# Kernel optimization log

Hardware: AMD Instinct MI355X
Metric: run time of the kernel (lower is better)

Reference implementation:

```python
import jax, jax.numpy as jnp
import numpy as np

EMBED_DIM = 2048
NUM_HEADS = 16
HEAD_DIM = EMBED_DIM // NUM_HEADS
BASE = 10000.0


def rotate_half(x):
    half = x.shape[-1] // 2
    x1, x2 = x[..., :half], x[..., half:]
    return jnp.concatenate([-x2, x1], axis=-1)


def apply_rope(x, base=BASE):
    # x: [B, H, S, Dh]
    S, Dh = x.shape[-2], x.shape[-1]
    inv_freq = 1.0 / (base ** (jnp.arange(0, Dh, 2, dtype=jnp.float32) / Dh))
    t = jnp.arange(S, dtype=jnp.float32)
    freqs = jnp.einsum('i,j->ij', t, inv_freq)          # [S, Dh/2]
    emb = jnp.concatenate([freqs, freqs], axis=-1)      # [S, Dh]
    return x * jnp.cos(emb) + rotate_half(x) * jnp.sin(emb)


def setup_inputs() -> dict:
    key = jax.random.key(0)
    ks = jax.random.split(key, 9)
    B, S, D = 2, 2048, EMBED_DIM
    xavier = lambda k, shape: jax.random.uniform(
        k, shape, jnp.float32, -1.0, 1.0) * float(np.sqrt(6.0 / (shape[0] + shape[1])))
    return {
        'x': jax.random.normal(ks[0], (B, S, D), jnp.float32),
        'q_w': xavier(ks[1], (D, D)),
        'k_w': xavier(ks[2], (D, D)),
        'v_w': xavier(ks[3], (D, D)),
        'q_b': jnp.zeros((D,), jnp.float32),
        'k_b': jnp.zeros((D,), jnp.float32),
        'v_b': jnp.zeros((D,), jnp.float32),
        'out_w': xavier(ks[4], (D, D)),
        'out_b': jnp.zeros((D,), jnp.float32),
    }


def reference(x, q_w, k_w, v_w, q_b, k_b, v_b, out_w, out_b):
    B, S, D = x.shape
    H, Dh = NUM_HEADS, HEAD_DIM
    scaling = Dh ** -0.5
    # F.linear(x, W, b) = x @ W.T + b
    q = (x @ q_w.T + q_b).reshape(B, S, H, Dh).transpose(0, 2, 1, 3)
    k = (x @ k_w.T + k_b).reshape(B, S, H, Dh).transpose(0, 2, 1, 3)
    v = (x @ v_w.T + v_b).reshape(B, S, H, Dh).transpose(0, 2, 1, 3)
    q = apply_rope(q)
    k = apply_rope(k)
    attn = jnp.einsum('bhqd,bhkd->bhqk', q, k) * scaling
    probs = jax.nn.softmax(attn, axis=-1)
    out = jnp.einsum('bhqk,bhkd->bhqd', probs, v)
    out = out.transpose(0, 2, 1, 3).reshape(B, S, D)
    return out @ out_w.T + out_b
```

## Files before the change

### kernel.cpp

```cpp
#include <hip/hip_runtime.h>
#include <stdint.h>

typedef __bf16 bf16;
typedef __bf16 bf16x4 __attribute__((ext_vector_type(4)));
typedef __bf16 bf16x8 __attribute__((ext_vector_type(8)));
typedef float f32x4 __attribute__((ext_vector_type(4)));

#define DM 2048
#define MM 4096
#define MFMA16(a, b, c) __builtin_amdgcn_mfma_f32_16x16x32_bf16(a, b, c, 0, 0, 0)

__device__ __forceinline__ void gload_lds16(const void* g, void* l) {
  __builtin_amdgcn_global_load_lds((const __attribute__((address_space(1))) uint32_t*)g,
                                   (__attribute__((address_space(3))) uint32_t*)l, 16, 0, 0);
}

__global__ __launch_bounds__(256) void cvt_f32_bf16(
    const float* __restrict__ s0, const float* __restrict__ s1,
    const float* __restrict__ s2, const float* __restrict__ s3,
    const float* __restrict__ s4,
    bf16* __restrict__ d0, bf16* __restrict__ d1, bf16* __restrict__ d2,
    bf16* __restrict__ d3, bf16* __restrict__ d4)
{
  const size_t i4 = (size_t)(blockIdx.x * 256 + threadIdx.x) * 4;
  const float* s; bf16* d; size_t off;
  if      (i4 <  8388608u) { s = s0; d = d0; off = i4;             }
  else if (i4 < 12582912u) { s = s1; d = d1; off = i4 -  8388608u; }
  else if (i4 < 16777216u) { s = s2; d = d2; off = i4 - 12582912u; }
  else if (i4 < 20971520u) { s = s3; d = d3; off = i4 - 16777216u; }
  else                     { s = s4; d = d4; off = i4 - 20971520u; }
  const float4 v = *(const float4*)(s + off);
  bf16x4 o = { (bf16)v.x, (bf16)v.y, (bf16)v.z, (bf16)v.w };
  *(bf16x4*)(d + off) = o;
}

__global__ __launch_bounds__(256, 2) void gemm_qkv_fused(
    const bf16* __restrict__ A,
    const bf16* __restrict__ Wq, const bf16* __restrict__ Wk, const bf16* __restrict__ Wv,
    const float* __restrict__ qb, const float* __restrict__ kb, const float* __restrict__ vb,
    bf16* __restrict__ Cq, bf16* __restrict__ Ck, bf16* __restrict__ Cv)
{
  __shared__ __align__(16) bf16 smem[32768];
  bf16* As = smem;
  bf16* Ws = smem + 8192;

  const int id = blockIdx.x;
  const int xcd = id & 7, jj = id >> 3;
  const int n0 = (xcd * 2 + (jj >> 5)) * 128;
  const int m0 = (jj & 31) * 128;

  const int t = threadIdx.x;
  const int wave = t >> 6, lane = t & 63;
  const int quad = lane >> 4, c16 = lane & 15;
  const int wr = wave >> 1, wc = wave & 1;

  f32x4 acc[3][4][4] = {};

  const int srow = t >> 3;
  const int scol = ((t & 7) ^ (srow & 7)) * 8;
  const bf16* gA  = A  + (size_t)(m0 + srow) * DM + scol;
  const bf16* gW0 = Wq + (size_t)(n0 + srow) * DM + scol;
  const bf16* gW1 = Wk + (size_t)(n0 + srow) * DM + scol;
  const bf16* gW2 = Wv + (size_t)(n0 + srow) * DM + scol;

  for (int k0 = 0; k0 < DM; k0 += 64) {
#pragma unroll
    for (int rr = 0; rr < 4; ++rr) {
      const size_t go = (size_t)(rr * 32) * DM;
      const int lo = (rr * 256 + wave * 64) * 8;
      gload_lds16(gA  + go, As + lo);
      gload_lds16(gW0 + go, Ws + lo);
      gload_lds16(gW1 + go, Ws + 8192 + lo);
      gload_lds16(gW2 + go, Ws + 16384 + lo);
    }
    gA += 64; gW0 += 64; gW1 += 64; gW2 += 64;
    __syncthreads();

#pragma unroll
    for (int ks = 0; ks < 2; ++ks) {
      bf16x8 af[4];
#pragma unroll
      for (int i = 0; i < 4; ++i) {
        const int row = wr * 64 + i * 16 + c16;
        const int gi = (ks * 4 + quad) ^ (row & 7);
        af[i] = *(const bf16x8*)&As[row * 64 + gi * 8];
      }
#pragma unroll
      for (int z = 0; z < 3; ++z) {
        bf16x8 bfr[4];
#pragma unroll
        for (int jx = 0; jx < 4; ++jx) {
          const int row = wc * 64 + jx * 16 + c16;
          const int gi = (ks * 4 + quad) ^ (row & 7);
          bfr[jx] = *(const bf16x8*)&Ws[z * 8192 + row * 64 + gi * 8];
        }
#pragma unroll
        for (int i = 0; i < 4; ++i)
#pragma unroll
          for (int jx = 0; jx < 4; ++jx)
            acc[z][i][jx] = MFMA16(af[i], bfr[jx], acc[z][i][jx]);
      }
    }
    __syncthreads();
  }

  const int h = n0 >> 7;
#pragma unroll
  for (int jx = 0; jx < 4; ++jx) {
    const int d = wc * 64 + jx * 16 + c16;
    const float bv = vb[n0 + d];
#pragma unroll
    for (int i = 0; i < 4; ++i) {
      const int row = m0 + wr * 64 + i * 16 + quad * 4;
      const int b = row >> 11, s = row & 2047;
      bf16x4 o;
#pragma unroll
      for (int r = 0; r < 4; ++r) o[r] = (bf16)(acc[2][i][jx][r] + bv);
      *(bf16x4*)&Cv[((size_t)((b * 16 + h) * 128 + d)) * 2048 + s] = o;
    }
  }

  bf16* Tl = smem;
#pragma unroll
  for (int z = 0; z < 2; ++z) {
    __syncthreads();
#pragma unroll
    for (int jx = 0; jx < 4; ++jx) {
      const int col = wc * 64 + jx * 16 + c16;
      const float bv = (z == 0 ? qb : kb)[n0 + col];
#pragma unroll
      for (int i = 0; i < 4; ++i) {
        const int row = wr * 64 + i * 16 + quad * 4;
#pragma unroll
        for (int r = 0; r < 4; ++r)
          Tl[(row + r) * 136 + col] = (bf16)(acc[z][i][jx][r] + bv);
      }
    }
    __syncthreads();
    bf16* C = (z == 0) ? Cq : Ck;
    const float scale = (z == 0) ? 0.08838834764831845f * 1.4426950408889634f : 1.0f;
#pragma unroll
    for (int rr = 0; rr < 4; ++rr) {
      const int row = rr * 32 + (t >> 3);
      const int d0 = (t & 7) * 8;
      const int s = (m0 + row) & 2047;
      bf16x8 xa = *(const bf16x8*)&Tl[row * 136 + d0];
      bf16x8 xb = *(const bf16x8*)&Tl[row * 136 + d0 + 64];
      bf16x8 o1, o2;
#pragma unroll
      for (int j = 0; j < 8; ++j) {
        const float inv_freq = __expf((float)(d0 + j) * -0.14391156514261228f);
        float sn, cs;
        __sincosf((float)s * inv_freq, &sn, &cs);
        const float a = (float)xa[j], bb = (float)xb[j];
        o1[j] = (bf16)((a * cs - bb * sn) * scale);
        o2[j] = (bf16)((bb * cs + a * sn) * scale);
      }
      *(bf16x8*)&C[(size_t)(m0 + row) * DM + n0 + d0]      = o1;
      *(bf16x8*)&C[(size_t)(m0 + row) * DM + n0 + d0 + 64] = o2;
    }
  }
}

__global__ __launch_bounds__(256, 2) void gemm_bias_f32(
    const bf16* __restrict__ A, const bf16* __restrict__ W,
    const float* __restrict__ bias, float* __restrict__ C)
{
  __shared__ __align__(16) bf16 As[8192];
  __shared__ __align__(16) bf16 Bs[8192];
  const int id = blockIdx.x;
  const int xcd = id & 7, jj = id >> 3;
  const int n0 = (xcd * 2 + (jj >> 5)) * 128;
  const int m0 = (jj & 31) * 128;

  const int t = threadIdx.x;
  const int wave = t >> 6, lane = t & 63;
  const int quad = lane >> 4, c16 = lane & 15;
  const int wr = wave >> 1, wc = wave & 1;

  f32x4 acc[4][4] = {};
  const int srow = t >> 3;
  const int scol = ((t & 7) ^ (srow & 7)) * 8;
  const bf16* gA = A + (size_t)(m0 + srow) * DM + scol;
  const bf16* gB = W + (size_t)(n0 + srow) * DM + scol;

  for (int k0 = 0; k0 < DM; k0 += 64) {
#pragma unroll
    for (int rr = 0; rr < 4; ++rr) {
      const size_t go = (size_t)(rr * 32) * DM;
      const int lo = (rr * 256 + wave * 64) * 8;
      gload_lds16(gA + go, As + lo);
      gload_lds16(gB + go, Bs + lo);
    }
    gA += 64; gB += 64;
    __syncthreads();

#pragma unroll
    for (int ks = 0; ks < 2; ++ks) {
      bf16x8 af[4], bfr[4];
#pragma unroll
      for (int i = 0; i < 4; ++i) {
        const int row = wr * 64 + i * 16 + c16;
        const int gi = (ks * 4 + quad) ^ (row & 7);
        af[i] = *(const bf16x8*)&As[row * 64 + gi * 8];
      }
#pragma unroll
      for (int jx = 0; jx < 4; ++jx) {
        const int row = wc * 64 + jx * 16 + c16;
        const int gi = (ks * 4 + quad) ^ (row & 7);
        bfr[jx] = *(const bf16x8*)&Bs[row * 64 + gi * 8];
      }
#pragma unroll
      for (int i = 0; i < 4; ++i)
#pragma unroll
        for (int jx = 0; jx < 4; ++jx)
          acc[i][jx] = MFMA16(af[i], bfr[jx], acc[i][jx]);
    }
    __syncthreads();
  }

#pragma unroll
  for (int jx = 0; jx < 4; ++jx) {
    const int col = n0 + wc * 64 + jx * 16 + c16;
    const float bv = bias[col];
#pragma unroll
    for (int i = 0; i < 4; ++i) {
      const int row = m0 + wr * 64 + i * 16 + quad * 4;
#pragma unroll
      for (int r = 0; r < 4; ++r)
        C[(size_t)(row + r) * DM + col] = acc[i][jx][r] + bv;
    }
  }
}

__global__ __launch_bounds__(256, 2) void attn(
    const bf16* __restrict__ Q, const bf16* __restrict__ K,
    const bf16* __restrict__ Vt, bf16* __restrict__ O)
{
  __shared__ __align__(16) bf16 Ks[2][4][32][32];
  __shared__ __align__(16) bf16 Vs[2][128][32];
  __shared__ __align__(16) bf16 Ps[4][2][16][40];
  const int t = threadIdx.x;
  const int wave = t >> 6, lane = t & 63;
  const int quad = lane >> 4, c16 = lane & 15;
  const int id = blockIdx.x;
  const int xcd = id & 7, jj = id >> 3;
  const int bh = xcd * 4 + (jj >> 4);
  const int q0 = (jj & 15) * 128;
  const int b = bh >> 4, h = bh & 15;

  bf16x8 qf[2][4];
#pragma unroll
  for (int g = 0; g < 2; ++g) {
    const bf16* qrow = Q + (size_t)(b * 2048 + q0 + wave * 32 + g * 16 + c16) * 2048
                         + (size_t)h * 128 + quad * 8;
#pragma unroll
    for (int ks = 0; ks < 4; ++ks) qf[g][ks] = *(const bf16x8*)(qrow + ks * 32);
  }

  float l_i[2] = {0.f, 0.f};
  f32x4 o_acc[2][8] = {};

  const bf16* Kg = K + (size_t)(b * 2048) * 2048 + (size_t)h * 128;
  const bf16* Vg = Vt + (size_t)bh * 128 * 2048;

  auto stage = [&](int kt0, int nb) {
#pragma unroll
    for (int rr = 0; rr < 2; ++rr) {
      const int g = rr * 256 + t;
      const int ks = g >> 7, krow = (g >> 2) & 31, c8 = g & 3;
      gload_lds16(Kg + (size_t)(kt0 + krow) * 2048 + ks * 32 + ((c8 ^ ((krow >> 1) & 3)) * 8),
                  (bf16*)Ks[nb] + (rr * 256 + wave * 64) * 8);
    }
#pragma unroll
    for (int rr = 0; rr < 2; ++rr) {
      const int g = rr * 256 + t;
      const int d = g >> 2, c8 = g & 3;
      gload_lds16(Vg + (size_t)d * 2048 + kt0 + ((c8 ^ ((d >> 1) & 3)) * 8),
                  (bf16*)Vs[nb] + (rr * 256 + wave * 64) * 8);
    }
  };

  stage(0, 0);
  __syncthreads();

#pragma unroll 2
  for (int kt = 0; kt < 64; ++kt) {
    const int cb = kt & 1;
    if (kt < 63) stage((kt + 1) * 32, cb ^ 1);

    f32x4 st[2][2] = {};
#pragma unroll
    for (int ks = 0; ks < 4; ++ks)
#pragma unroll
      for (int nt = 0; nt < 2; ++nt) {
        const int row = nt * 16 + c16;
        bf16x8 kf = *(const bf16x8*)&Ks[cb][ks][row][(quad ^ ((row >> 1) & 3)) * 8];
        st[0][nt] = MFMA16(kf, qf[0][ks], st[0][nt]);
        st[1][nt] = MFMA16(kf, qf[1][ks], st[1][nt]);
      }

#pragma unroll
    for (int g = 0; g < 2; ++g) {
      float ps = 0.f;
#pragma unroll
      for (int nt = 0; nt < 2; ++nt) {
        bf16x4 pk;
#pragma unroll
        for (int r = 0; r < 4; ++r) {
          const float p = exp2f(st[g][nt][r]);
          ps += p;
          pk[r] = (bf16)p;
        }
        *(bf16x4*)&Ps[wave][g][c16][nt * 16 + quad * 4] = pk;
      }
      l_i[g] += ps;
    }

    bf16x8 pf0 = *(const bf16x8*)&Ps[wave][0][c16][quad * 8];
    bf16x8 pf1 = *(const bf16x8*)&Ps[wave][1][c16][quad * 8];
#pragma unroll
    for (int dt = 0; dt < 8; ++dt) {
      const int row = dt * 16 + c16;
      bf16x8 vf = *(const bf16x8*)&Vs[cb][row][(quad ^ ((row >> 1) & 3)) * 8];
      o_acc[0][dt] = MFMA16(vf, pf0, o_acc[0][dt]);
      o_acc[1][dt] = MFMA16(vf, pf1, o_acc[1][dt]);
    }

    __syncthreads();
  }

#pragma unroll
  for (int g = 0; g < 2; ++g) {
    float l = l_i[g];
    l += __shfl_xor(l, 16, 64);
    l += __shfl_xor(l, 32, 64);
    const float invl = 1.0f / l;
    const int qrow = q0 + wave * 32 + g * 16 + c16;
    bf16* orow = O + (size_t)(b * 2048 + qrow) * 2048 + (size_t)h * 128 + quad * 4;
#pragma unroll
    for (int dt = 0; dt < 8; ++dt) {
      bf16x4 o;
#pragma unroll
      for (int r = 0; r < 4; ++r) o[r] = (bf16)(o_acc[g][dt][r] * invl);
      *(bf16x4*)(orow + dt * 16) = o;
    }
  }
}

extern "C" void kernel_launch(void* const* d_in, const int* in_sizes, int n_in,
                              void* d_out, int out_size, void* d_ws, size_t ws_size,
                              hipStream_t stream)
{
  (void)in_sizes; (void)n_in; (void)out_size; (void)ws_size;
  const float* x   = (const float*)d_in[0];
  const float* q_w = (const float*)d_in[1];
  const float* k_w = (const float*)d_in[2];
  const float* v_w = (const float*)d_in[3];
  const float* q_b = (const float*)d_in[4];
  const float* k_b = (const float*)d_in[5];
  const float* v_b = (const float*)d_in[6];
  const float* o_w = (const float*)d_in[7];
  const float* o_b = (const float*)d_in[8];

  const size_t NELEM = (size_t)MM * DM;
  const size_t WELEM = (size_t)DM * DM;
  bf16* Xb  = (bf16*)d_ws;
  bf16* Wq  = Xb + NELEM;
  bf16* Wk  = Wq + WELEM;
  bf16* Wv  = Wk + WELEM;
  bf16* Wo  = Wv + WELEM;
  bf16* Q   = Wo + WELEM;
  bf16* Kb  = Q  + NELEM;
  bf16* Vt  = Kb + NELEM;
  bf16* attnO = Xb;

  cvt_f32_bf16<<<24576, 256, 0, stream>>>(x, q_w, k_w, v_w, o_w, Xb, Wq, Wk, Wv, Wo);

  gemm_qkv_fused<<<512, 256, 0, stream>>>(Xb, Wq, Wk, Wv, q_b, k_b, v_b, Q, Kb, Vt);
  attn<<<512, 256, 0, stream>>>(Q, Kb, Vt, attnO);
  gemm_bias_f32<<<512, 256, 0, stream>>>(attnO, Wo, o_b, (float*)d_out);
}
```

Measured before the change: 369.6 us.

## Switch attention to 32x32 MFMA with register-resident P and 64-key tiles

The attention kernel now uses 32x32x16 bf16 MFMAs instead of 16x16x32, and each wave handles 32 query rows with a single f32x16 accumulator set. The probability tile is packed with v_cvt_pk_bf16_f32 and rearranged across lanes with v_permlane32_swap, which removes the LDS round-trip for P. The key tile grows from 32 to 64 per iteration, halving the number of barriers, and the LDS swizzle changes to match. The larger K/V buffers raise LDS use, and the hand-written lane permutation is a correctness risk.

```diff
diff --git a/kernel.cpp b/kernel.cpp
--- a/kernel.cpp
+++ b/kernel.cpp
@@ -5,10 +5,12 @@
 typedef __bf16 bf16x4 __attribute__((ext_vector_type(4)));
 typedef __bf16 bf16x8 __attribute__((ext_vector_type(8)));
 typedef float f32x4 __attribute__((ext_vector_type(4)));
+typedef float f32x16 __attribute__((ext_vector_type(16)));
 
 #define DM 2048
 #define MM 4096
 #define MFMA16(a, b, c) __builtin_amdgcn_mfma_f32_16x16x32_bf16(a, b, c, 0, 0, 0)
+#define MFMA32(a, b, c) __builtin_amdgcn_mfma_f32_32x32x16_bf16(a, b, c, 0, 0, 0)
 
 __device__ __forceinline__ void gload_lds16(const void* g, void* l) {
   __builtin_amdgcn_global_load_lds((const __attribute__((address_space(1))) uint32_t*)g,
@@ -237,46 +239,44 @@
     const bf16* __restrict__ Q, const bf16* __restrict__ K,
     const bf16* __restrict__ Vt, bf16* __restrict__ O)
 {
-  __shared__ __align__(16) bf16 Ks[2][4][32][32];
-  __shared__ __align__(16) bf16 Vs[2][128][32];
-  __shared__ __align__(16) bf16 Ps[4][2][16][40];
+  __shared__ __align__(16) bf16 Ks[2][64][128];
+  __shared__ __align__(16) bf16 Vs[2][128][64];
   const int t = threadIdx.x;
   const int wave = t >> 6, lane = t & 63;
-  const int quad = lane >> 4, c16 = lane & 15;
+  const int r31 = lane & 31, h = lane >> 5;
   const int id = blockIdx.x;
   const int xcd = id & 7, jj = id >> 3;
   const int bh = xcd * 4 + (jj >> 4);
   const int q0 = (jj & 15) * 128;
-  const int b = bh >> 4, h = bh & 15;
-
-  bf16x8 qf[2][4];
-#pragma unroll
-  for (int g = 0; g < 2; ++g) {
-    const bf16* qrow = Q + (size_t)(b * 2048 + q0 + wave * 32 + g * 16 + c16) * 2048
-                         + (size_t)h * 128 + quad * 8;
-#pragma unroll
-    for (int ks = 0; ks < 4; ++ks) qf[g][ks] = *(const bf16x8*)(qrow + ks * 32);
-  }
-
-  float l_i[2] = {0.f, 0.f};
-  f32x4 o_acc[2][8] = {};
-
-  const bf16* Kg = K + (size_t)(b * 2048) * 2048 + (size_t)h * 128;
+  const int b = bh >> 4, hd = bh & 15;
+
+  bf16x8 qf[8];
+  {
+    const bf16* qrow = Q + (size_t)(b * 2048 + q0 + wave * 32 + r31) * 2048
+                         + (size_t)hd * 128 + h * 8;
+#pragma unroll
+    for (int ks = 0; ks < 8; ++ks) qf[ks] = *(const bf16x8*)(qrow + ks * 16);
+  }
+
+  float l_i = 0.f;
+  f32x16 o_acc[4] = {};
+
+  const bf16* Kg = K + (size_t)(b * 2048) * 2048 + (size_t)hd * 128;
   const bf16* Vg = Vt + (size_t)bh * 128 * 2048;
 
   auto stage = [&](int kt0, int nb) {
 #pragma unroll
-    for (int rr = 0; rr < 2; ++rr) {
-      const int g = rr * 256 + t;
-      const int ks = g >> 7, krow = (g >> 2) & 31, c8 = g & 3;
-      gload_lds16(Kg + (size_t)(kt0 + krow) * 2048 + ks * 32 + ((c8 ^ ((krow >> 1) & 3)) * 8),
+    for (int rr = 0; rr < 4; ++rr) {
+      const int G = rr * 256 + t;
+      const int key = G >> 4, gl = G & 15;
+      gload_lds16(Kg + (size_t)(kt0 + key) * 2048 + ((gl ^ (key & 7)) * 8),
                   (bf16*)Ks[nb] + (rr * 256 + wave * 64) * 8);
     }
 #pragma unroll
-    for (int rr = 0; rr < 2; ++rr) {
-      const int g = rr * 256 + t;
-      const int d = g >> 2, c8 = g & 3;
-      gload_lds16(Vg + (size_t)d * 2048 + kt0 + ((c8 ^ ((d >> 1) & 3)) * 8),
+    for (int rr = 0; rr < 4; ++rr) {
+      const int G = rr * 256 + t;
+      const int d = G >> 3, gl = G & 7;
+      gload_lds16(Vg + (size_t)d * 2048 + kt0 + ((gl ^ (d & 7)) * 8),
                   (bf16*)Vs[nb] + (rr * 256 + wave * 64) * 8);
     }
   };
@@ -285,67 +285,69 @@
   __syncthreads();
 
 #pragma unroll 2
-  for (int kt = 0; kt < 64; ++kt) {
+  for (int kt = 0; kt < 32; ++kt) {
     const int cb = kt & 1;
-    if (kt < 63) stage((kt + 1) * 32, cb ^ 1);
-
-    f32x4 st[2][2] = {};
-#pragma unroll
-    for (int ks = 0; ks < 4; ++ks)
-#pragma unroll
-      for (int nt = 0; nt < 2; ++nt) {
-        const int row = nt * 16 + c16;
-        bf16x8 kf = *(const bf16x8*)&Ks[cb][ks][row][(quad ^ ((row >> 1) & 3)) * 8];
-        st[0][nt] = MFMA16(kf, qf[0][ks], st[0][nt]);
-        st[1][nt] = MFMA16(kf, qf[1][ks], st[1][nt]);
-      }
-
-#pragma unroll
-    for (int g = 0; g < 2; ++g) {
-      float ps = 0.f;
-#pragma unroll
-      for (int nt = 0; nt < 2; ++nt) {
-        bf16x4 pk;
-#pragma unroll
-        for (int r = 0; r < 4; ++r) {
-          const float p = exp2f(st[g][nt][r]);
-          ps += p;
-          pk[r] = (bf16)p;
+    if (kt < 31) stage((kt + 1) * 64, cb ^ 1);
+
+#pragma unroll
+    for (int rb = 0; rb < 2; ++rb) {
+      f32x16 st = {};
+#pragma unroll
+      for (int ks = 0; ks < 8; ++ks) {
+        const int key = rb * 32 + r31;
+        const int g = (2 * ks + h) ^ (key & 7);
+        bf16x8 kf = *(const bf16x8*)&Ks[cb][key][g * 8];
+        st = MFMA32(kf, qf[ks], st);
+      }
+
+      float p[16];
+#pragma unroll
+      for (int r = 0; r < 16; ++r) { p[r] = exp2f(st[r]); l_i += p[r]; }
+
+      uint32_t pka[4], pkb[4];
+#pragma unroll
+      for (int pp = 0; pp < 4; ++pp) {
+        asm("v_cvt_pk_bf16_f32 %0, %1, %2"
+            : "=v"(pka[pp]) : "v"(p[4 * pp + 0]), "v"(p[4 * pp + 1]));
+        asm("v_cvt_pk_bf16_f32 %0, %1, %2"
+            : "=v"(pkb[pp]) : "v"(p[4 * pp + 2]), "v"(p[4 * pp + 3]));
+      }
+
+#pragma unroll
+      for (int c = 0; c < 2; ++c) {
+        uint32_t a0 = pka[2 * c], a1 = pka[2 * c + 1];
+        uint32_t b0 = pkb[2 * c], b1 = pkb[2 * c + 1];
+        asm("v_permlane32_swap_b32 %0, %1" : "+v"(a0), "+v"(a1));
+        asm("v_permlane32_swap_b32 %0, %1" : "+v"(b0), "+v"(b1));
+        union { uint32_t u[4]; bf16x8 v; } pf;
+        pf.u[0] = a0; pf.u[1] = b0; pf.u[2] = a1; pf.u[3] = b1;
+        const int kap = rb * 2 + c;
+#pragma unroll
+        for (int db = 0; db < 4; ++db) {
+          const int d = db * 32 + r31;
+          const int g = (2 * kap + h) ^ (d & 7);
+          bf16x8 vf = *(const bf16x8*)&Vs[cb][d][g * 8];
+          o_acc[db] = MFMA32(vf, pf.v, o_acc[db]);
         }
-        *(bf16x4*)&Ps[wave][g][c16][nt * 16 + quad * 4] = pk;
-      }
-      l_i[g] += ps;
-    }
-
-    bf16x8 pf0 = *(const bf16x8*)&Ps[wave][0][c16][quad * 8];
-    bf16x8 pf1 = *(const bf16x8*)&Ps[wave][1][c16][quad * 8];
-#pragma unroll
-    for (int dt = 0; dt < 8; ++dt) {
-      const int row = dt * 16 + c16;
-      bf16x8 vf = *(const bf16x8*)&Vs[cb][row][(quad ^ ((row >> 1) & 3)) * 8];
-      o_acc[0][dt] = MFMA16(vf, pf0, o_acc[0][dt]);
-      o_acc[1][dt] = MFMA16(vf, pf1, o_acc[1][dt]);
-    }
-
-    __syncthreads();
-  }
-
-#pragma unroll
-  for (int g = 0; g < 2; ++g) {
-    float l = l_i[g];
-    l += __shfl_xor(l, 16, 64);
-    l += __shfl_xor(l, 32, 64);
-    const float invl = 1.0f / l;
-    const int qrow = q0 + wave * 32 + g * 16 + c16;
-    bf16* orow = O + (size_t)(b * 2048 + qrow) * 2048 + (size_t)h * 128 + quad * 4;
-#pragma unroll
-    for (int dt = 0; dt < 8; ++dt) {
+      }
+    }
+    __syncthreads();
+  }
+
+  l_i += __shfl_xor(l_i, 32, 64);
+  const float invl = 1.0f / l_i;
+  const int q = q0 + wave * 32 + r31;
+  bf16* orow = O + (size_t)(b * 2048 + q) * 2048 + (size_t)hd * 128;
+#pragma unroll
+  for (int db = 0; db < 4; ++db)
+#pragma unroll
+    for (int pp = 0; pp < 4; ++pp) {
+      const int d0 = db * 32 + 8 * pp + 4 * h;
       bf16x4 o;
 #pragma unroll
-      for (int r = 0; r < 4; ++r) o[r] = (bf16)(o_acc[g][dt][r] * invl);
-      *(bf16x4*)(orow + dt * 16) = o;
-    }
-  }
+      for (int r = 0; r < 4; ++r) o[r] = (bf16)(o_acc[db][4 * pp + r] * invl);
+      *(bf16x4*)(orow + d0) = o;
+    }
 }
 
 extern "C" void kernel_launch(void* const* d_in, const int* in_sizes, int n_in,
```

New measurement: 364.4 us. About the same (-1.4%).
